# Optimization experiments

Measured on AMD Instinct MI355X. Metric: run time of the kernel, lower is better.

## Reference

```python
import jax, jax.numpy as jnp
import numpy as np

B, V, M, C = 1024, 2, 256, 256  # batch, num_vars (must be 2), latent states, categories


def setup_inputs() -> dict:
    key = jax.random.key(0)
    k1, k2, k3 = jax.random.split(key, 3)
    x = jax.random.randint(k1, (B, V), 0, C)
    # input-node tables: per var v, per latent node k, a [M, C] row-normalized table
    W = jax.nn.softmax(jax.random.normal(k2, (V, M, M, C), dtype=jnp.float32), axis=-1)
    # sum-node mixture weights over the M product children
    w_sum = jax.nn.softmax(jax.random.normal(k3, (M,), dtype=jnp.float32))
    return {"x": x, "W": W, "w_sum": w_sum}


def reference(x, W, w_sum):
    # lp[v] has shape [M(k), M(m), B]: log W[v, k, m, x[b, v]]
    # (matches torch: probs[:, x_var].log() per input node, stacked over latent k)
    lp0 = jnp.log(W[0][:, :, x[:, 0]])  # [M, M, B]
    lp1 = jnp.log(W[1][:, :, x[:, 1]])  # [M, M, B]
    prod = lp0 + lp1                    # product nodes, [M(k), M, B]
    # sum node: log( sum_k w_k * exp(prod_k) ) -> [M, B]
    mixed = jnp.log(jnp.einsum('k,kmb->mb', w_sum, jnp.exp(prod)))
    # root: logsumexp over the leading M dim -> [B]
    return jax.nn.logsumexp(mixed, axis=0)
```

## Files before the change

### kernel.cpp

```cpp
#include <hip/hip_runtime.h>
#include <hip/hip_bf16.h>
#include <math.h>


#define NC       256
#define KKTOT    65536
#define SPLITS   128
#define KCHUNK   512
#define BK       32
#define LDS_STRIDE 40

typedef float  f32x4  __attribute__((ext_vector_type(4)));
typedef short  bf16x8 __attribute__((ext_vector_type(8)));

static __device__ __forceinline__ short f2bf(float f) {
    unsigned u = __builtin_bit_cast(unsigned, f);
    u += 0x7fffu + ((u >> 16) & 1u);
    return (short)(u >> 16);
}

template <bool USE_PART>
__global__ __launch_bounds__(256, 2) void gemm_s_kernel(
    const float* __restrict__ W, const float* __restrict__ wsum,
    float* __restrict__ out_acc)
{
    __shared__ short As[128 * LDS_STRIDE];
    __shared__ short Bs[128 * LDS_STRIDE];

    const int tile   = blockIdx.x;
    const int split  = blockIdx.y;
    const int c0base = (tile >> 1) * 128;
    const int c1base = (tile & 1) * 128;
    const long kbase = (long)split * KCHUNK;

    const float* __restrict__ Ag = W;
    const float* __restrict__ Bg = W + 16777216;

    const int t  = threadIdx.x;
    const int cq = t & 31;
    const int kq = t >> 5;

    const int lane = t & 63;
    const int wv   = t >> 6;
    const int wc0  = (wv >> 1) * 64;
    const int wc1  = (wv & 1) * 64;
    const int ml   = lane & 15;
    const int qd   = lane >> 4;

    f32x4 acc[4][4];
#pragma unroll
    for (int i = 0; i < 4; ++i)
#pragma unroll
        for (int j = 0; j < 4; ++j) acc[i][j] = (f32x4){0.f, 0.f, 0.f, 0.f};

    for (int it = 0; it < KCHUNK / BK; ++it) {
        const long k0 = kbase + (long)it * BK;
        float4 a4[4], b4[4];
        float  wsc[4];
#pragma unroll
        for (int r = 0; r < 4; ++r) {
            const long kk = k0 + kq * 4 + r;
            wsc[r] = wsum[kk >> 8];
            a4[r]  = *(const float4*)(Ag + kk * 256 + (c0base + cq * 4));
            b4[r]  = *(const float4*)(Bg + kk * 256 + (c1base + cq * 4));
        }
        __syncthreads();
        const float* af32 = reinterpret_cast<const float*>(a4);
        const float* bf32 = reinterpret_cast<const float*>(b4);
#pragma unroll
        for (int j = 0; j < 4; ++j) {
            short4 av, bv;
            av.x = f2bf(af32[0 * 4 + j] * wsc[0]);
            av.y = f2bf(af32[1 * 4 + j] * wsc[1]);
            av.z = f2bf(af32[2 * 4 + j] * wsc[2]);
            av.w = f2bf(af32[3 * 4 + j] * wsc[3]);
            bv.x = f2bf(bf32[0 * 4 + j]);
            bv.y = f2bf(bf32[1 * 4 + j]);
            bv.z = f2bf(bf32[2 * 4 + j]);
            bv.w = f2bf(bf32[3 * 4 + j]);
            const int c = cq * 4 + j;
            *(short4*)&As[c * LDS_STRIDE + kq * 4] = av;
            *(short4*)&Bs[c * LDS_STRIDE + kq * 4] = bv;
        }
        __syncthreads();
        bf16x8 af[4], bf[4];
#pragma unroll
        for (int mi = 0; mi < 4; ++mi)
            af[mi] = *(const bf16x8*)&As[(wc0 + mi * 16 + ml) * LDS_STRIDE + qd * 8];
#pragma unroll
        for (int ni = 0; ni < 4; ++ni)
            bf[ni] = *(const bf16x8*)&Bs[(wc1 + ni * 16 + ml) * LDS_STRIDE + qd * 8];
#pragma unroll
        for (int mi = 0; mi < 4; ++mi)
#pragma unroll
            for (int ni = 0; ni < 4; ++ni)
                acc[mi][ni] = __builtin_amdgcn_mfma_f32_16x16x32_bf16(
                    af[mi], bf[ni], acc[mi][ni], 0, 0, 0);
    }

    if (USE_PART) {
        float* __restrict__ Pb = out_acc + ((size_t)split * 4 + tile) * 16384;
#pragma unroll
        for (int mi = 0; mi < 4; ++mi) {
            const int row0 = wc0 + mi * 16 + qd * 4;
#pragma unroll
            for (int ni = 0; ni < 4; ++ni) {
                const int col = wc1 + ni * 16 + ml;
#pragma unroll
                for (int r = 0; r < 4; ++r)
                    Pb[(row0 + r) * 128 + col] = acc[mi][ni][r];
            }
        }
    } else {
#pragma unroll
        for (int mi = 0; mi < 4; ++mi) {
            const int row0 = c0base + wc0 + mi * 16 + qd * 4;
#pragma unroll
            for (int ni = 0; ni < 4; ++ni) {
                const int col = c1base + wc1 + ni * 16 + ml;
#pragma unroll
                for (int r = 0; r < 4; ++r)
                    atomicAdd(&out_acc[(row0 + r) * 256 + col], acc[mi][ni][r]);
            }
        }
    }
}

__global__ __launch_bounds__(64) void finish_part_kernel(
    const int* __restrict__ x, const float* __restrict__ P, float* __restrict__ out)
{
    const int b  = blockIdx.x;
    const int t  = threadIdx.x;
    const int x0 = x[2 * b], x1 = x[2 * b + 1];
    const int tile  = ((x0 >> 7) << 1) | (x1 >> 7);
    const int local = ((x0 & 127) << 7) | (x1 & 127);
    float v = P[((size_t)(t) * 4 + tile) * 16384 + local]
            + P[((size_t)(t + 64) * 4 + tile) * 16384 + local];
#pragma unroll
    for (int off = 32; off > 0; off >>= 1) v += __shfl_down(v, off);
    if (t == 0) out[b] = logf(v);
}

__global__ __launch_bounds__(64) void finish_atom_kernel(
    const int* __restrict__ x, const float* __restrict__ S, float* __restrict__ out)
{
    const int b = blockIdx.x * 64 + threadIdx.x;
    const int x0 = x[2 * b], x1 = x[2 * b + 1];
    out[b] = logf(S[x0 * 256 + x1]);
}

extern "C" void kernel_launch(void* const* d_in, const int* in_sizes, int n_in,
                              void* d_out, int out_size, void* d_ws, size_t ws_size,
                              hipStream_t stream)
{
    const int*   x    = (const int*)d_in[0];
    const float* W    = (const float*)d_in[1];
    const float* wsum = (const float*)d_in[2];
    float* out = (float*)d_out;

    const size_t part_bytes = (size_t)SPLITS * 4 * 16384 * sizeof(float);

    if (ws_size >= part_bytes) {
        float* P = (float*)d_ws;
        gemm_s_kernel<true><<<dim3(4, SPLITS), 256, 0, stream>>>(W, wsum, P);
        finish_part_kernel<<<dim3(1024), 64, 0, stream>>>(x, P, out);
    } else {
        float* S = (float*)d_ws;
        hipMemsetAsync(d_ws, 0, 65536 * sizeof(float), stream);
        gemm_s_kernel<false><<<dim3(4, SPLITS), 256, 0, stream>>>(W, wsum, S);
        finish_atom_kernel<<<dim3(16), 64, 0, stream>>>(x, S, out);
    }
}
```

Before: 212.6 us.

## Enlarge GEMM tile to 256x128 with 512 threads to halve A reloads

Each block now covers the full 256 rows of the A side and one 128-column half of B, using 8 waves instead of 4. Previously A was loaded twice, once per c1 tile. The grid drops from 4x128 to 2x128 blocks. The per-k scaling by wsum is hoisted to two scalars per split, since each 512-row chunk spans exactly two latent nodes. The cost is fewer blocks (256 on a 256-CU part), more LDS and more register pressure per block.

```diff
diff --git a/kernel.cpp b/kernel.cpp
--- a/kernel.cpp
+++ b/kernel.cpp
@@ -1,14 +1,12 @@
 #include <hip/hip_runtime.h>
-#include <hip/hip_bf16.h>
 #include <math.h>
 
 
-#define NC       256
-#define KKTOT    65536
-#define SPLITS   128
-#define KCHUNK   512
-#define BK       32
-#define LDS_STRIDE 40
+#define SPLITS  128
+#define KCHUNK  512
+#define BK      32
+#define NITER   (KCHUNK / BK)
+#define LDSS    40
 
 typedef float  f32x4  __attribute__((ext_vector_type(4)));
 typedef short  bf16x8 __attribute__((ext_vector_type(8)));
@@ -20,32 +18,35 @@
 }
 
 template <bool USE_PART>
-__global__ __launch_bounds__(256, 2) void gemm_s_kernel(
+__global__ __launch_bounds__(512, 2) void gemm_s_kernel(
     const float* __restrict__ W, const float* __restrict__ wsum,
     float* __restrict__ out_acc)
 {
-    __shared__ short As[128 * LDS_STRIDE];
-    __shared__ short Bs[128 * LDS_STRIDE];
+    __shared__ short As[256 * LDSS];
+    __shared__ short Bs[128 * LDSS];
 
-    const int tile   = blockIdx.x;
-    const int split  = blockIdx.y;
-    const int c0base = (tile >> 1) * 128;
-    const int c1base = (tile & 1) * 128;
-    const long kbase = (long)split * KCHUNK;
+    const int  c1tile = blockIdx.x;
+    const int  split  = blockIdx.y;
+    const long kbase  = (long)split * KCHUNK;
 
     const float* __restrict__ Ag = W;
-    const float* __restrict__ Bg = W + 16777216;
+    const float* __restrict__ Bg = W + 16777216 + (long)c1tile * 128;
 
-    const int t  = threadIdx.x;
-    const int cq = t & 31;
-    const int kq = t >> 5;
+    const int t = threadIdx.x;
+    const int cqA = (t & 63) * 4;
+    const int kqA = (t >> 6) * 4;
+    const int cqB = (t & 31) * 4;
+    const int kqB = (t >> 5) * 2;
 
     const int lane = t & 63;
     const int wv   = t >> 6;
-    const int wc0  = (wv >> 1) * 64;
-    const int wc1  = (wv & 1) * 64;
+    const int wc0  = (wv & 3) * 64;
+    const int wc1  = (wv >> 2) * 64;
     const int ml   = lane & 15;
     const int qd   = lane >> 4;
+
+    const float w0 = wsum[split * 2];
+    const float w1 = wsum[split * 2 + 1];
 
     f32x4 acc[4][4];
 #pragma unroll
@@ -53,53 +54,49 @@
 #pragma unroll
         for (int j = 0; j < 4; ++j) acc[i][j] = (f32x4){0.f, 0.f, 0.f, 0.f};
 
-    for (int it = 0; it < KCHUNK / BK; ++it) {
-        const long k0 = kbase + (long)it * BK;
-        float4 a4[4], b4[4];
-        float  wsc[4];
+    for (int it = 0; it < NITER; ++it) {
+        const long  k0 = kbase + (long)it * BK;
+        const float wk = (it < NITER / 2) ? w0 : w1;
+        float4 a4[4], b4[2];
 #pragma unroll
-        for (int r = 0; r < 4; ++r) {
-            const long kk = k0 + kq * 4 + r;
-            wsc[r] = wsum[kk >> 8];
-            a4[r]  = *(const float4*)(Ag + kk * 256 + (c0base + cq * 4));
-            b4[r]  = *(const float4*)(Bg + kk * 256 + (c1base + cq * 4));
-        }
+        for (int r = 0; r < 4; ++r)
+            a4[r] = *(const float4*)(Ag + (k0 + kqA + r) * 256 + cqA);
+#pragma unroll
+        for (int r = 0; r < 2; ++r)
+            b4[r] = *(const float4*)(Bg + (k0 + kqB + r) * 256 + cqB);
         __syncthreads();
         const float* af32 = reinterpret_cast<const float*>(a4);
         const float* bf32 = reinterpret_cast<const float*>(b4);
 #pragma unroll
         for (int j = 0; j < 4; ++j) {
-            short4 av, bv;
-            av.x = f2bf(af32[0 * 4 + j] * wsc[0]);
-            av.y = f2bf(af32[1 * 4 + j] * wsc[1]);
-            av.z = f2bf(af32[2 * 4 + j] * wsc[2]);
-            av.w = f2bf(af32[3 * 4 + j] * wsc[3]);
+            short4 av;
+            av.x = f2bf(af32[0 * 4 + j] * wk);
+            av.y = f2bf(af32[1 * 4 + j] * wk);
+            av.z = f2bf(af32[2 * 4 + j] * wk);
+            av.w = f2bf(af32[3 * 4 + j] * wk);
+            *(short4*)&As[(cqA + j) * LDSS + kqA] = av;
+            short2 bv;
             bv.x = f2bf(bf32[0 * 4 + j]);
             bv.y = f2bf(bf32[1 * 4 + j]);
-            bv.z = f2bf(bf32[2 * 4 + j]);
-            bv.w = f2bf(bf32[3 * 4 + j]);
-            const int c = cq * 4 + j;
-            *(short4*)&As[c * LDS_STRIDE + kq * 4] = av;
-            *(short4*)&Bs[c * LDS_STRIDE + kq * 4] = bv;
+            *(short2*)&Bs[(cqB + j) * LDSS + kqB] = bv;
         }
         __syncthreads();
-        bf16x8 af[4], bf[4];
+        bf16x8 afr[4];
 #pragma unroll
         for (int mi = 0; mi < 4; ++mi)
-            af[mi] = *(const bf16x8*)&As[(wc0 + mi * 16 + ml) * LDS_STRIDE + qd * 8];
+            afr[mi] = *(const bf16x8*)&As[(wc0 + mi * 16 + ml) * LDSS + qd * 8];
 #pragma unroll
-        for (int ni = 0; ni < 4; ++ni)
-            bf[ni] = *(const bf16x8*)&Bs[(wc1 + ni * 16 + ml) * LDS_STRIDE + qd * 8];
+        for (int ni = 0; ni < 4; ++ni) {
+            const bf16x8 bfr = *(const bf16x8*)&Bs[(wc1 + ni * 16 + ml) * LDSS + qd * 8];
 #pragma unroll
-        for (int mi = 0; mi < 4; ++mi)
-#pragma unroll
-            for (int ni = 0; ni < 4; ++ni)
+            for (int mi = 0; mi < 4; ++mi)
                 acc[mi][ni] = __builtin_amdgcn_mfma_f32_16x16x32_bf16(
-                    af[mi], bf[ni], acc[mi][ni], 0, 0, 0);
+                    afr[mi], bfr, acc[mi][ni], 0, 0, 0);
+        }
     }
 
     if (USE_PART) {
-        float* __restrict__ Pb = out_acc + ((size_t)split * 4 + tile) * 16384;
+        float* __restrict__ Pb = out_acc + ((size_t)split * 2 + c1tile) * 32768;
 #pragma unroll
         for (int mi = 0; mi < 4; ++mi) {
             const int row0 = wc0 + mi * 16 + qd * 4;
@@ -114,10 +111,10 @@
     } else {
 #pragma unroll
         for (int mi = 0; mi < 4; ++mi) {
-            const int row0 = c0base + wc0 + mi * 16 + qd * 4;
+            const int row0 = wc0 + mi * 16 + qd * 4;
 #pragma unroll
             for (int ni = 0; ni < 4; ++ni) {
-                const int col = c1base + wc1 + ni * 16 + ml;
+                const int col = c1tile * 128 + wc1 + ni * 16 + ml;
 #pragma unroll
                 for (int r = 0; r < 4; ++r)
                     atomicAdd(&out_acc[(row0 + r) * 256 + col], acc[mi][ni][r]);
@@ -132,10 +129,10 @@
     const int b  = blockIdx.x;
     const int t  = threadIdx.x;
     const int x0 = x[2 * b], x1 = x[2 * b + 1];
-    const int tile  = ((x0 >> 7) << 1) | (x1 >> 7);
-    const int local = ((x0 & 127) << 7) | (x1 & 127);
-    float v = P[((size_t)(t) * 4 + tile) * 16384 + local]
-            + P[((size_t)(t + 64) * 4 + tile) * 16384 + local];
+    const int t1 = x1 >> 7;
+    const size_t base = (size_t)x0 * 128 + (x1 & 127);
+    float v = P[((size_t)t * 2 + t1) * 32768 + base]
+            + P[((size_t)(t + 64) * 2 + t1) * 32768 + base];
 #pragma unroll
     for (int off = 32; off > 0; off >>= 1) v += __shfl_down(v, off);
     if (t == 0) out[b] = logf(v);
@@ -144,7 +141,7 @@
 __global__ __launch_bounds__(64) void finish_atom_kernel(
     const int* __restrict__ x, const float* __restrict__ S, float* __restrict__ out)
 {
-    const int b = blockIdx.x * 64 + threadIdx.x;
+    const int b  = blockIdx.x * 64 + threadIdx.x;
     const int x0 = x[2 * b], x1 = x[2 * b + 1];
     out[b] = logf(S[x0 * 256 + x1]);
 }
@@ -158,16 +155,16 @@
     const float* wsum = (const float*)d_in[2];
     float* out = (float*)d_out;
 
-    const size_t part_bytes = (size_t)SPLITS * 4 * 16384 * sizeof(float);
+    const size_t part_bytes = (size_t)SPLITS * 2 * 32768 * sizeof(float);
 
     if (ws_size >= part_bytes) {
         float* P = (float*)d_ws;
-        gemm_s_kernel<true><<<dim3(4, SPLITS), 256, 0, stream>>>(W, wsum, P);
+        gemm_s_kernel<true><<<dim3(2, SPLITS), 512, 0, stream>>>(W, wsum, P);
         finish_part_kernel<<<dim3(1024), 64, 0, stream>>>(x, P, out);
     } else {
         float* S = (float*)d_ws;
         hipMemsetAsync(d_ws, 0, 65536 * sizeof(float), stream);
-        gemm_s_kernel<false><<<dim3(4, SPLITS), 256, 0, stream>>>(W, wsum, S);
+        gemm_s_kernel<false><<<dim3(2, SPLITS), 512, 0, stream>>>(W, wsum, S);
         finish_atom_kernel<<<dim3(16), 64, 0, stream>>>(x, S, out);
     }
 }
```

New measurement: 208.9 us. No clear change (-1.8%).
